# Kernel tuning notes

Hardware: AMD Instinct MI355X
Metric: run time of the kernel (lower is better)

Reference implementation:

```python
import jax, jax.numpy as jnp
import numpy as np

# ---- module config (from init_kwargs) ----
KERNEL_SIZE = 3
DIM = 3
HALF = KERNEL_SIZE // 2          # kernel offsets span [-HALF, HALF]
COORD_RANGE = 256                # voxel grid extent per spatial axis
NUM_BATCH = 4
N_VOXELS = 100_000
FEAT_DIM = 32
STRIDE = COORD_RANGE + 2 * HALF  # encoding stride so shifted coords fit


def _kernel_offsets():
    # All offsets of a KERNEL_SIZE^DIM kernel, centered (MinkowskiEngine-style).
    r = np.arange(-HALF, HALF + 1)
    grids = np.meshgrid(*([r] * DIM), indexing='ij')
    return jnp.asarray(np.stack([g.ravel() for g in grids], axis=1), dtype=jnp.int32)  # [K, DIM]


def setup_inputs() -> dict:
    key = jax.random.key(0)
    k1, k2, k3 = jax.random.split(key, 3)
    batch = jax.random.randint(k1, (1, N_VOXELS), 0, NUM_BATCH, dtype=jnp.int32)
    coords = jax.random.randint(k2, (3, N_VOXELS), 0, COORD_RANGE, dtype=jnp.int32)
    sparse_indices = jnp.concatenate([batch, coords], axis=0)  # [4, N]
    features = jax.random.normal(k3, (N_VOXELS, FEAT_DIM), dtype=jnp.float32)
    return {"sparse_indices": sparse_indices, "features": features}


def _kernel_map_and_out_key(sparse_indices):
    offsets = _kernel_offsets()                 # [K, 3]
    K = offsets.shape[0]
    b = sparse_indices[0].astype(jnp.int32)     # [N]
    coords = sparse_indices[1:].T.astype(jnp.int32)  # [N, 3]
    N = coords.shape[0]
    NK = N * K

    # neighbor coords per (voxel, offset); shift by HALF so values are >= 0
    nbr = coords[:, None, :] + offsets[None, :, :] + HALF     # [N, K, 3]
    S = STRIDE
    # unique integer hash of (batch, x, y, z); fits in int32 for these ranges
    enc = ((b[:, None] * S + nbr[..., 0]) * S + nbr[..., 1]) * S + nbr[..., 2]
    enc = enc.reshape(-1)                                     # [NK]

    # unique keys (sorted) + inverse map; pad to static size NK
    uniq, inv = jnp.unique(enc, return_inverse=True, size=NK, fill_value=-1)

    # reorder unique keys into first-seen order to match the dict-based reference
    first = jnp.full((NK,), NK, dtype=jnp.int32).at[inv].min(
        jnp.arange(NK, dtype=jnp.int32))
    order = jnp.argsort(first)                                # padding sorts last
    new_id = jnp.zeros((NK,), dtype=jnp.int32).at[order].set(
        jnp.arange(NK, dtype=jnp.int32))
    out_idx = new_id[inv]                                     # [NK] output index per entry

    # decode unique (first-seen ordered) keys back to spatial coords
    uo = uniq[order]
    valid = uo >= 0
    z = uo % S
    y = (uo // S) % S
    x = (uo // (S * S)) % S
    out_key = jnp.stack([x, y, z], axis=1) - HALF             # undo shift
    out_key = jnp.where(valid[:, None], out_key, -1)          # [NK, 3], padded rows = -1

    input_idx = jnp.repeat(jnp.arange(N, dtype=jnp.int32), K) # [NK]
    rel_pos = jnp.tile(jnp.arange(K, dtype=jnp.int32), N)     # [NK]
    kernel_map = jnp.stack([input_idx, out_idx, rel_pos], axis=1)  # [NK, 3]
    return kernel_map, out_key


def reference(sparse_indices, features):
    kernel_map, out_key = _kernel_map_and_out_key(sparse_indices)
    NK = kernel_map.shape[0]
    # canonical downstream use of the kernel map: gather inputs, scatter-sum to outputs
    out_feats = jax.ops.segment_sum(features[kernel_map[:, 0]],
                                    kernel_map[:, 1], num_segments=NK)
    return kernel_map, out_key, out_feats
```

## Files before the change

kernel.cpp:

```cpp
#include <hip/hip_runtime.h>
#include <stdint.h>

typedef unsigned long long u64;
typedef unsigned u32;
typedef float __attribute__((ext_vector_type(4))) f4raw;

#define K 27
#define S 258
#define ENCMAX (4 * S * S * S)

__device__ __forceinline__ void gbar(int* cnt, int nblk) {
    __syncthreads();
    if (threadIdx.x == 0) {
        __threadfence();
        __hip_atomic_fetch_add(cnt, 1, __ATOMIC_RELEASE, __HIP_MEMORY_SCOPE_AGENT);
        while (__hip_atomic_load(cnt, __ATOMIC_RELAXED, __HIP_MEMORY_SCOPE_AGENT) < nblk)
            __builtin_amdgcn_s_sleep(2);
        (void)__hip_atomic_load(cnt, __ATOMIC_ACQUIRE, __HIP_MEMORY_SCOPE_AGENT);
        __threadfence();
    }
    __syncthreads();
}

__global__ void k_mark(const int* __restrict__ si, int N,
                       u64* __restrict__ bits, u64* __restrict__ dupb) {
    int idx = blockIdx.x * blockDim.x + threadIdx.x;
    if (idx >= N * 9) return;
    int n = idx / 9, run = idx - n * 9;
    int ox = run / 3, oy = run - ox * 3;
    int b = si[n], x = si[N + n], y = si[2 * N + n], z = si[3 * N + n];
    unsigned enc0 = (unsigned)(((b * S + x + ox) * S + (y + oy)) * S + z);
    unsigned w = enc0 >> 6; int bit = enc0 & 63;
    u64 m1 = 7ull << bit;
    u64 old = atomicOr(&bits[w], m1);
    u64 d1 = old & m1;
    if (d1) atomicOr(&dupb[w], d1);
    if (bit > 61) {
        u64 m2 = 7ull >> (64 - bit);
        u64 old2 = atomicOr(&bits[w + 1], m2);
        u64 d2 = old2 & m2;
        if (d2) atomicOr(&dupb[w + 1], d2);
    }
}

__global__ void __launch_bounds__(256, 2)
k_s13(const u64* __restrict__ bits, const u64* __restrict__ dupb,
      int* __restrict__ tsums, u32* __restrict__ wprefix,
      int* __restrict__ minE, int NK, int* __restrict__ barcnt) {
    __shared__ int s[256];
    __shared__ int tb;
    int tid = threadIdx.x;
    int b = blockIdx.x;
    int gs = gridDim.x * 256;
    for (int i = b * 256 + tid; i < NK; i += gs) minE[i] = 0x7F7F7F7F;

    size_t wb = (size_t)b * 4096 + (size_t)tid * 16;
    int pc[16]; int tsum = 0;
#pragma unroll
    for (int j = 0; j < 16; j++) { pc[j] = __popcll(bits[wb + j]); tsum += pc[j]; }
    s[tid] = tsum; __syncthreads();
    for (int off = 128; off > 0; off >>= 1) {
        if (tid < off) s[tid] += s[tid + off];
        __syncthreads();
    }
    if (tid == 0) tsums[b] = s[0];
    gbar(barcnt, gridDim.x);
    int pre = 0;
    for (int j = tid; j < b; j += 256) pre += tsums[j];
    s[tid] = pre; __syncthreads();
    for (int off = 128; off > 0; off >>= 1) {
        if (tid < off) s[tid] += s[tid + off];
        __syncthreads();
    }
    if (tid == 0) tb = s[0];
    __syncthreads();
    int tbase = tb;
    s[tid] = tsum; __syncthreads();
    for (int off = 1; off < 256; off <<= 1) {
        int t = (tid >= off) ? s[tid - off] : 0;
        __syncthreads();
        s[tid] += t;
        __syncthreads();
    }
    int run = tbase + s[tid] - tsum;
#pragma unroll
    for (int j = 0; j < 16; j++) {
        u32 dup = (dupb[wb + j] != 0ull) ? 0x80000000u : 0u;
        wprefix[wb + j] = (u32)run | dup;
        run += pc[j];
    }
}

__global__ void k_kid(const int* __restrict__ si, int N,
                      const u64* __restrict__ bits, const u64* __restrict__ dupb,
                      const u32* __restrict__ wprefix,
                      int* __restrict__ kid, int* __restrict__ minE) {
    int idx = blockIdx.x * blockDim.x + threadIdx.x;
    if (idx >= N * 9) return;
    int n = idx / 9, run = idx - n * 9;
    int ox = run / 3, oy = run - ox * 3;
    int b = si[n], x = si[N + n], y = si[2 * N + n], z = si[3 * N + n];
    unsigned enc0 = (unsigned)(((b * S + x + ox) * S + (y + oy)) * S + z);
    unsigned w = enc0 >> 6; int bit = enc0 & 63;
    u64 bw0 = bits[w]; u32 q0 = wprefix[w];
    u64 db0 = (q0 & 0x80000000u) ? dupb[w] : 0ull;
    u64 bw1 = 0, db1 = 0; u32 q1 = 0;
    if (bit > 61) {
        bw1 = bits[w + 1]; q1 = wprefix[w + 1];
        db1 = (q1 & 0x80000000u) ? dupb[w + 1] : 0ull;
    }
    int e0 = n * K + run * 3;
#pragma unroll
    for (int oz = 0; oz < 3; ++oz) {
        unsigned enc = enc0 + oz;
        int bit2 = enc & 63;
        bool hi = (enc >> 6) != w;
        u64 bwx = hi ? bw1 : bw0;
        u64 dbx = hi ? db1 : db0;
        u32 q   = hi ? q1 : q0;
        int kd = (int)(q & 0x7FFFFFFFu) + __popcll(bwx & ((1ull << bit2) - 1));
        int multi = (int)((dbx >> bit2) & 1);
        kid[e0 + oz] = multi ? (int)((u32)kd | 0x80000000u) : kd;
        if (multi) atomicMin(&minE[kd], e0 + oz);
    }
}

__global__ void k_flagsum(const int* __restrict__ kid, const int* __restrict__ minE,
                          int NK, int* __restrict__ bsums) {
    __shared__ int s[256];
    int tid = threadIdx.x;
    int base = blockIdx.x * 4096 + tid * 16;
    int kv[16];
    *(int4*)(kv + 0)  = *(const int4*)(kid + base + 0);
    *(int4*)(kv + 4)  = *(const int4*)(kid + base + 4);
    *(int4*)(kv + 8)  = *(const int4*)(kid + base + 8);
    *(int4*)(kv + 12) = *(const int4*)(kid + base + 12);
    int sum = 0;
#pragma unroll
    for (int j = 0; j < 16; j++) {
        int e = base + j;
        if (e < NK) {
            int v = kv[j];
            sum += (v >= 0) ? 1 : (minE[v & 0x7FFFFFFF] == e ? 1 : 0);
        }
    }
    s[tid] = sum; __syncthreads();
    for (int off = 128; off > 0; off >>= 1) {
        if (tid < off) s[tid] += s[tid + off];
        __syncthreads();
    }
    if (tid == 0) bsums[blockIdx.x] = s[0];
}

__global__ void k_scanC(int* __restrict__ kid, const int* __restrict__ minE,
                        const int* __restrict__ bsums, const int* __restrict__ si,
                        int N, int NK, int NB,
                        float* __restrict__ out_key, int* __restrict__ rank_key,
                        float4* __restrict__ outF4) {
    __shared__ int s[256];
    __shared__ u64 s2[256];
    int tid = threadIdx.x;
    u64 acc = 0;
    for (int j = tid; j < NB; j += 256) {
        u64 b = (u64)(u32)bsums[j];
        acc += b << 32;
        if (j < (int)blockIdx.x) acc += b;
    }
    s2[tid] = acc; __syncthreads();
    for (int off = 128; off > 0; off >>= 1) {
        if (tid < off) s2[tid] += s2[tid + off];
        __syncthreads();
    }
    int blockoff = (int)(u32)(s2[0] & 0xFFFFFFFFull);
    int U = (int)(s2[0] >> 32);

    int base = blockIdx.x * 4096 + tid * 16;
    int kv[16];
    *(int4*)(kv + 0)  = *(const int4*)(kid + base + 0);
    *(int4*)(kv + 4)  = *(const int4*)(kid + base + 4);
    *(int4*)(kv + 8)  = *(const int4*)(kid + base + 8);
    *(int4*)(kv + 12) = *(const int4*)(kid + base + 12);
    int fbits = 0;
#pragma unroll
    for (int j = 0; j < 16; j++) {
        int e = base + j;
        int f = 0;
        if (e < NK) {
            int v = kv[j];
            f = (v >= 0) ? 1 : (minE[v & 0x7FFFFFFF] == e ? 1 : 0);
        }
        fbits |= f << j;
    }
    int tsum = __popc(fbits);
    s[tid] = tsum; __syncthreads();
    for (int off = 1; off < 256; off <<= 1) {
        int t = (tid >= off) ? s[tid - off] : 0;
        __syncthreads();
        s[tid] += t;
        __syncthreads();
    }
    int offset = blockoff + s[tid] - tsum;
    float4 zf = {0.f, 0.f, 0.f, 0.f};
    int run = 0;
#pragma unroll
    for (int j = 0; j < 16; j++) {
        int e = base + j;
        if ((fbits >> j) & 1) {
            int rank = offset + run;
            int n = e / K; int m = e - n * K;
            int x = si[N + n], y = si[2 * N + n], z = si[3 * N + n];
            int ox = m / 9; int rm = m - ox * 9; int oy = rm / 3; int oz = rm - oy * 3;
            out_key[(size_t)rank * 3 + 0] = (float)(x + ox - 1);
            out_key[(size_t)rank * 3 + 1] = (float)(y + oy - 1);
            out_key[(size_t)rank * 3 + 2] = (float)(z + oz - 1);
            int v = kv[j];
            if (v < 0) {
                int kd = v & 0x7FFFFFFF;
                rank_key[kd] = rank;
                kid[e] = rank | 0x40000000;
                float4* q = outF4 + (size_t)rank * 8;
#pragma unroll
                for (int q8 = 0; q8 < 8; q8++) q[q8] = zf;
            } else {
                kid[e] = rank;
            }
            run++;
        }
    }
    int rows = NK - U;
    int gs = gridDim.x * blockDim.x;
    for (int i = blockIdx.x * blockDim.x + tid; i < rows; i += gs) {
        int row = U + i;
        float4* q = outF4 + (size_t)row * 8;
#pragma unroll
        for (int q8 = 0; q8 < 8; q8++) q[q8] = zf;
        out_key[(size_t)row * 3 + 0] = -1.0f;
        out_key[(size_t)row * 3 + 1] = -1.0f;
        out_key[(size_t)row * 3 + 2] = -1.0f;
    }
}

__global__ void k_final(const int* __restrict__ ent, const int* __restrict__ rank_key,
                        const float4* __restrict__ feat4,
                        float* __restrict__ km, float* __restrict__ outF, int NK) {
    int total = NK * 8;
    int gs = gridDim.x * blockDim.x;
    for (int idx = blockIdx.x * blockDim.x + threadIdx.x; idx < total; idx += gs) {
        int e = idx >> 3, g = idx & 7;
        int v = ent[e];
        int n = e / K, m = e - n * K;
        float4 val = feat4[(size_t)n * 8 + g];
        int uid, atom;
        if (v < 0)                { uid = rank_key[v & 0x7FFFFFFF]; atom = 1; }
        else if (v & 0x40000000)  { uid = v & 0x3FFFFFFF;           atom = 1; }
        else                      { uid = v;                        atom = 0; }
        float* dst = outF + (size_t)uid * 32 + g * 4;
        if (atom) {
            atomicAdd(dst + 0, val.x);
            atomicAdd(dst + 1, val.y);
            atomicAdd(dst + 2, val.z);
            atomicAdd(dst + 3, val.w);
        } else {
            f4raw vr = {val.x, val.y, val.z, val.w};
            __builtin_nontemporal_store(vr, (f4raw*)dst);
        }
        if (g < 3)
            km[(size_t)e * 3 + g] = (g == 0) ? (float)n
                                   : ((g == 1) ? (float)uid : (float)m);
    }
}

extern "C" void kernel_launch(void* const* d_in, const int* in_sizes, int n_in,
                              void* d_out, int out_size, void* d_ws, size_t ws_size,
                              hipStream_t stream) {
    const int* si = (const int*)d_in[0];
    const float4* feat4 = (const float4*)d_in[1];
    int N = in_sizes[0] / 4;
    int NK = N * K;
    int NKp = (NK + 4095) & ~4095;
    int NB = NKp / 4096;

    int NW = (ENCMAX + 63) / 64;
    int NT = (NW + 4095) / 4096;
    int NWp = NT * 4096;

    float* km = (float*)d_out;
    float* out_key = km + (size_t)NK * 3;
    float* outF = km + (size_t)NK * 6;

    char* w = (char*)d_ws;
    char* p_bar   = w; w += 64;
    char* p_bits  = w; w += ((size_t)NWp * 8 + 15) & ~(size_t)15;
    char* p_dupb  = w; w += ((size_t)NWp * 8 + 15) & ~(size_t)15;
    size_t zbytes = (size_t)(w - (char*)d_ws);
    char* p_tsums = w; w += ((size_t)(NT + 1) * 4 + 15) & ~(size_t)15;
    char* p_wpref = w; w += ((size_t)NWp * 4 + 15) & ~(size_t)15;
    char* p_minE  = w; w += ((size_t)NK * 4 + 15) & ~(size_t)15;
    char* p_kid   = w; w += ((size_t)NKp * 4 + 15) & ~(size_t)15;
    char* p_rank  = w; w += ((size_t)NK * 4 + 15) & ~(size_t)15;
    char* p_bsums = w; w += ((size_t)(NB + 1) * 4 + 15) & ~(size_t)15;

    int* barcnt   = (int*)p_bar;
    u64* bits     = (u64*)p_bits;
    u64* dupb     = (u64*)p_dupb;
    int* tsums    = (int*)p_tsums;
    u32* wprefix  = (u32*)p_wpref;
    int* minE     = (int*)p_minE;
    int* kid      = (int*)p_kid;
    int* rank_key = (int*)p_rank;
    int* bsums    = (int*)p_bsums;

    (void)hipMemsetAsync(d_ws, 0, zbytes, stream);

    int nb9 = (N * 9 + 255) / 256;
    k_mark<<<nb9, 256, 0, stream>>>(si, N, bits, dupb);
    k_s13<<<NT, 256, 0, stream>>>(bits, dupb, tsums, wprefix, minE, NK, barcnt);
    k_kid<<<nb9, 256, 0, stream>>>(si, N, bits, dupb, wprefix, kid, minE);
    k_flagsum<<<NB, 256, 0, stream>>>(kid, minE, NK, bsums);
    k_scanC<<<NB, 256, 0, stream>>>(kid, minE, bsums, si, N, NK, NB,
                                    out_key, rank_key, (float4*)outF);
    k_final<<<2048, 256, 0, stream>>>(kid, rank_key, feat4, km, outF, NK);
}
```

Measured before the change: 601.4 us.

## Compact duplicate entries and fuse flag counting into kid and scan kernels

k_kid now accumulates per-tile counts of unique entries directly into bsums and appends duplicate-key entries to a compact list. A small pass, folded into k_scanC behind a grid barrier when the grid fits, resolves each duplicate's first occurrence into a dupfirst bitmask. This removes the separate full k_flagsum pass and the minE lookups in the scan. The cost is extra atomics, a software grid barrier that assumes all NB blocks are co-resident (launch_bounds 256,3), and a larger k_final grid.

Result: slower. 727.9 us (+21.0%).

```diff
diff --git a/kernel.cpp b/kernel.cpp
--- a/kernel.cpp
+++ b/kernel.cpp
@@ -94,92 +94,127 @@
 __global__ void k_kid(const int* __restrict__ si, int N,
                       const u64* __restrict__ bits, const u64* __restrict__ dupb,
                       const u32* __restrict__ wprefix,
-                      int* __restrict__ kid, int* __restrict__ minE) {
-    int idx = blockIdx.x * blockDim.x + threadIdx.x;
-    if (idx >= N * 9) return;
-    int n = idx / 9, run = idx - n * 9;
-    int ox = run / 3, oy = run - ox * 3;
-    int b = si[n], x = si[N + n], y = si[2 * N + n], z = si[3 * N + n];
-    unsigned enc0 = (unsigned)(((b * S + x + ox) * S + (y + oy)) * S + z);
-    unsigned w = enc0 >> 6; int bit = enc0 & 63;
-    u64 bw0 = bits[w]; u32 q0 = wprefix[w];
-    u64 db0 = (q0 & 0x80000000u) ? dupb[w] : 0ull;
-    u64 bw1 = 0, db1 = 0; u32 q1 = 0;
-    if (bit > 61) {
-        bw1 = bits[w + 1]; q1 = wprefix[w + 1];
-        db1 = (q1 & 0x80000000u) ? dupb[w + 1] : 0ull;
-    }
-    int e0 = n * K + run * 3;
-#pragma unroll
-    for (int oz = 0; oz < 3; ++oz) {
-        unsigned enc = enc0 + oz;
-        int bit2 = enc & 63;
-        bool hi = (enc >> 6) != w;
-        u64 bwx = hi ? bw1 : bw0;
-        u64 dbx = hi ? db1 : db0;
-        u32 q   = hi ? q1 : q0;
-        int kd = (int)(q & 0x7FFFFFFFu) + __popcll(bwx & ((1ull << bit2) - 1));
-        int multi = (int)((dbx >> bit2) & 1);
-        kid[e0 + oz] = multi ? (int)((u32)kd | 0x80000000u) : kd;
-        if (multi) atomicMin(&minE[kd], e0 + oz);
-    }
-}
-
-__global__ void k_flagsum(const int* __restrict__ kid, const int* __restrict__ minE,
-                          int NK, int* __restrict__ bsums) {
+                      int* __restrict__ kid, int* __restrict__ minE,
+                      int* __restrict__ duplist, int* __restrict__ dupcnt,
+                      int* __restrict__ bsums) {
+    __shared__ int sc0, sc1, lcnt, lbase;
+    int tid = threadIdx.x;
+    if (tid == 0) { sc0 = 0; sc1 = 0; lcnt = 0; }
+    __syncthreads();
+    int idx = blockIdx.x * 256 + tid;
+    int mye[3]; int myslot[3]; int mycnt = 0;
+    int s0 = 0, s1 = 0;
+    int t0 = (blockIdx.x * 768) >> 12;
+    if (idx < N * 9) {
+        int n = idx / 9, run = idx - n * 9;
+        int ox = run / 3, oy = run - ox * 3;
+        int b = si[n], x = si[N + n], y = si[2 * N + n], z = si[3 * N + n];
+        unsigned enc0 = (unsigned)(((b * S + x + ox) * S + (y + oy)) * S + z);
+        unsigned w = enc0 >> 6; int bit = enc0 & 63;
+        u64 bw0 = bits[w]; u32 q0 = wprefix[w];
+        u64 db0 = (q0 & 0x80000000u) ? dupb[w] : 0ull;
+        u64 bw1 = 0, db1 = 0; u32 q1 = 0;
+        if (bit > 61) {
+            bw1 = bits[w + 1]; q1 = wprefix[w + 1];
+            db1 = (q1 & 0x80000000u) ? dupb[w + 1] : 0ull;
+        }
+        int e0 = idx * 3;
+#pragma unroll
+        for (int oz = 0; oz < 3; ++oz) {
+            unsigned enc = enc0 + oz;
+            int bit2 = enc & 63;
+            bool hi = (enc >> 6) != w;
+            u64 bwx = hi ? bw1 : bw0;
+            u64 dbx = hi ? db1 : db0;
+            u32 q   = hi ? q1 : q0;
+            int kd = (int)(q & 0x7FFFFFFFu) + __popcll(bwx & ((1ull << bit2) - 1));
+            int multi = (int)((dbx >> bit2) & 1);
+            int e = e0 + oz;
+            if (multi) {
+                kid[e] = (int)((u32)kd | 0x80000000u);
+                atomicMin(&minE[kd], e);
+                myslot[mycnt] = atomicAdd(&lcnt, 1);
+                mye[mycnt] = e;
+                mycnt++;
+            } else {
+                kid[e] = kd;
+                if ((e >> 12) == t0) s0++; else s1++;
+            }
+        }
+    }
+    if (s0) atomicAdd(&sc0, s0);
+    if (s1) atomicAdd(&sc1, s1);
+    __syncthreads();
+    if (tid == 0) {
+        if (lcnt) lbase = atomicAdd(dupcnt, lcnt);
+        if (sc0) atomicAdd(&bsums[t0], sc0);
+        if (sc1) atomicAdd(&bsums[t0 + 1], sc1);
+    }
+    __syncthreads();
+    for (int i = 0; i < mycnt; i++) duplist[lbase + myslot[i]] = mye[i];
+}
+
+__global__ void k_flagB(const int* __restrict__ duplist, const int* __restrict__ dupcnt,
+                        const int* __restrict__ kid, const int* __restrict__ minE,
+                        u32* __restrict__ dupfirst, int* __restrict__ bsums) {
+    int M = *dupcnt;
+    int gs = gridDim.x * blockDim.x;
+    for (int i = blockIdx.x * blockDim.x + threadIdx.x; i < M; i += gs) {
+        int e = duplist[i];
+        int kd = kid[e] & 0x7FFFFFFF;
+        if (minE[kd] == e) {
+            atomicOr(&dupfirst[e >> 5], 1u << (e & 31));
+            atomicAdd(&bsums[e >> 12], 1);
+        }
+    }
+}
+
+__global__ void __launch_bounds__(256, 3)
+k_scanC(int* __restrict__ kid, const int* __restrict__ duplist,
+        const int* __restrict__ dupcnt, const int* __restrict__ minE,
+        u32* __restrict__ dupfirst, int* __restrict__ bsums,
+        const int* __restrict__ si, int N, int NK, int NB, int fused,
+        float* __restrict__ out_key, int* __restrict__ rank_key,
+        float4* __restrict__ outF4, int* __restrict__ barcnt) {
     __shared__ int s[256];
+    __shared__ u64 s2[256];
     int tid = threadIdx.x;
-    int base = blockIdx.x * 4096 + tid * 16;
+    int b = blockIdx.x;
+    if (fused) {
+        int M = *dupcnt;
+        int gs = gridDim.x * 256;
+        for (int i = b * 256 + tid; i < M; i += gs) {
+            int e = duplist[i];
+            int kd = kid[e] & 0x7FFFFFFF;
+            if (minE[kd] == e) {
+                atomicOr(&dupfirst[e >> 5], 1u << (e & 31));
+                atomicAdd(&bsums[e >> 12], 1);
+            }
+        }
+        gbar(barcnt, gridDim.x);
+    }
+    u64 acc = 0;
+    for (int j = tid; j < NB; j += 256) {
+        u64 v = (u64)(u32)bsums[j];
+        acc += v << 32;
+        if (j < b) acc += v;
+    }
+    s2[tid] = acc; __syncthreads();
+    for (int off = 128; off > 0; off >>= 1) {
+        if (tid < off) s2[tid] += s2[tid + off];
+        __syncthreads();
+    }
+    int blockoff = (int)(u32)(s2[0] & 0xFFFFFFFFull);
+    int U = (int)(s2[0] >> 32);
+
+    int base = b * 4096 + tid * 16;
     int kv[16];
     *(int4*)(kv + 0)  = *(const int4*)(kid + base + 0);
     *(int4*)(kv + 4)  = *(const int4*)(kid + base + 4);
     *(int4*)(kv + 8)  = *(const int4*)(kid + base + 8);
     *(int4*)(kv + 12) = *(const int4*)(kid + base + 12);
-    int sum = 0;
-#pragma unroll
-    for (int j = 0; j < 16; j++) {
-        int e = base + j;
-        if (e < NK) {
-            int v = kv[j];
-            sum += (v >= 0) ? 1 : (minE[v & 0x7FFFFFFF] == e ? 1 : 0);
-        }
-    }
-    s[tid] = sum; __syncthreads();
-    for (int off = 128; off > 0; off >>= 1) {
-        if (tid < off) s[tid] += s[tid + off];
-        __syncthreads();
-    }
-    if (tid == 0) bsums[blockIdx.x] = s[0];
-}
-
-__global__ void k_scanC(int* __restrict__ kid, const int* __restrict__ minE,
-                        const int* __restrict__ bsums, const int* __restrict__ si,
-                        int N, int NK, int NB,
-                        float* __restrict__ out_key, int* __restrict__ rank_key,
-                        float4* __restrict__ outF4) {
-    __shared__ int s[256];
-    __shared__ u64 s2[256];
-    int tid = threadIdx.x;
-    u64 acc = 0;
-    for (int j = tid; j < NB; j += 256) {
-        u64 b = (u64)(u32)bsums[j];
-        acc += b << 32;
-        if (j < (int)blockIdx.x) acc += b;
-    }
-    s2[tid] = acc; __syncthreads();
-    for (int off = 128; off > 0; off >>= 1) {
-        if (tid < off) s2[tid] += s2[tid + off];
-        __syncthreads();
-    }
-    int blockoff = (int)(u32)(s2[0] & 0xFFFFFFFFull);
-    int U = (int)(s2[0] >> 32);
-
-    int base = blockIdx.x * 4096 + tid * 16;
-    int kv[16];
-    *(int4*)(kv + 0)  = *(const int4*)(kid + base + 0);
-    *(int4*)(kv + 4)  = *(const int4*)(kid + base + 4);
-    *(int4*)(kv + 8)  = *(const int4*)(kid + base + 8);
-    *(int4*)(kv + 12) = *(const int4*)(kid + base + 12);
+    u32 dupw = dupfirst[base >> 5];
+    int bits16 = (int)((dupw >> ((tid & 1) * 16)) & 0xFFFFu);
     int fbits = 0;
 #pragma unroll
     for (int j = 0; j < 16; j++) {
@@ -187,7 +222,7 @@
         int f = 0;
         if (e < NK) {
             int v = kv[j];
-            f = (v >= 0) ? 1 : (minE[v & 0x7FFFFFFF] == e ? 1 : 0);
+            f = (v >= 0) ? 1 : ((bits16 >> j) & 1);
         }
         fbits |= f << j;
     }
@@ -228,8 +263,8 @@
         }
     }
     int rows = NK - U;
-    int gs = gridDim.x * blockDim.x;
-    for (int i = blockIdx.x * blockDim.x + tid; i < rows; i += gs) {
+    int gs2 = gridDim.x * blockDim.x;
+    for (int i = b * 256 + tid; i < rows; i += gs2) {
         int row = U + i;
         float4* q = outF4 + (size_t)row * 8;
 #pragma unroll
@@ -292,32 +327,44 @@
     char* p_bar   = w; w += 64;
     char* p_bits  = w; w += ((size_t)NWp * 8 + 15) & ~(size_t)15;
     char* p_dupb  = w; w += ((size_t)NWp * 8 + 15) & ~(size_t)15;
+    char* p_dupf  = w; w += ((size_t)(NKp / 8) + 15) & ~(size_t)15;
+    char* p_bsums = w; w += ((size_t)(NB + 1) * 4 + 15) & ~(size_t)15;
+    char* p_cnt   = w; w += 16;
     size_t zbytes = (size_t)(w - (char*)d_ws);
     char* p_tsums = w; w += ((size_t)(NT + 1) * 4 + 15) & ~(size_t)15;
     char* p_wpref = w; w += ((size_t)NWp * 4 + 15) & ~(size_t)15;
     char* p_minE  = w; w += ((size_t)NK * 4 + 15) & ~(size_t)15;
     char* p_kid   = w; w += ((size_t)NKp * 4 + 15) & ~(size_t)15;
     char* p_rank  = w; w += ((size_t)NK * 4 + 15) & ~(size_t)15;
-    char* p_bsums = w; w += ((size_t)(NB + 1) * 4 + 15) & ~(size_t)15;
+    char* p_dlist = w; w += ((size_t)NK * 4 + 15) & ~(size_t)15;
 
     int* barcnt   = (int*)p_bar;
     u64* bits     = (u64*)p_bits;
     u64* dupb     = (u64*)p_dupb;
+    u32* dupfirst = (u32*)p_dupf;
+    int* bsums    = (int*)p_bsums;
+    int* dupcnt   = (int*)p_cnt;
     int* tsums    = (int*)p_tsums;
     u32* wprefix  = (u32*)p_wpref;
     int* minE     = (int*)p_minE;
     int* kid      = (int*)p_kid;
     int* rank_key = (int*)p_rank;
-    int* bsums    = (int*)p_bsums;
+    int* duplist  = (int*)p_dlist;
 
     (void)hipMemsetAsync(d_ws, 0, zbytes, stream);
 
     int nb9 = (N * 9 + 255) / 256;
     k_mark<<<nb9, 256, 0, stream>>>(si, N, bits, dupb);
     k_s13<<<NT, 256, 0, stream>>>(bits, dupb, tsums, wprefix, minE, NK, barcnt);
-    k_kid<<<nb9, 256, 0, stream>>>(si, N, bits, dupb, wprefix, kid, minE);
-    k_flagsum<<<NB, 256, 0, stream>>>(kid, minE, NK, bsums);
-    k_scanC<<<NB, 256, 0, stream>>>(kid, minE, bsums, si, N, NK, NB,
-                                    out_key, rank_key, (float4*)outF);
-    k_final<<<2048, 256, 0, stream>>>(kid, rank_key, feat4, km, outF, NK);
-}
+    k_kid<<<nb9, 256, 0, stream>>>(si, N, bits, dupb, wprefix, kid, minE,
+                                   duplist, dupcnt, bsums);
+    int fused = (NB <= 768) ? 1 : 0;
+    if (!fused)
+        k_flagB<<<256, 256, 0, stream>>>(duplist, dupcnt, kid, minE,
+                                         dupfirst, bsums);
+    k_scanC<<<NB, 256, 0, stream>>>(kid, duplist, dupcnt, minE, dupfirst,
+                                    bsums, si, N, NK, NB, fused,
+                                    out_key, rank_key, (float4*)outF,
+                                    barcnt + 1);
+    k_final<<<4096, 256, 0, stream>>>(kid, rank_key, feat4, km, outF, NK);
+}
```
